# Kernel tuning notes

Hardware: AMD Instinct MI355X
Metric: run time of the kernel (lower is better)

Reference implementation:

```python
import jax, jax.numpy as jnp
import numpy as np

N = 100000
E = 1600000
IN_C = 128
HID = 64


def setup_inputs() -> dict:
    key = jax.random.key(0)
    ks = jax.random.split(key, 8)
    x = jax.random.normal(ks[0], (N, IN_C), dtype=jnp.float32)
    edge_index = jax.random.randint(ks[1], (2, E), 0, N, dtype=jnp.int64)
    # Glorot-ish init for faithfulness; exact init values don't matter for correctness baseline
    W1 = jax.random.normal(ks[2], (IN_C, HID), dtype=jnp.float32) / np.sqrt(IN_C)
    b1 = jnp.zeros((HID,), dtype=jnp.float32)
    W2 = jax.random.normal(ks[3], (HID, HID), dtype=jnp.float32) / np.sqrt(HID)
    b2 = jnp.zeros((HID,), dtype=jnp.float32)
    Wc = jax.random.normal(ks[4], (HID, 1), dtype=jnp.float32) / np.sqrt(HID)
    bc = jnp.zeros((1,), dtype=jnp.float32)
    return {"x": x, "edge_index": edge_index, "W1": W1, "b1": b1,
            "W2": W2, "b2": b2, "Wc": Wc, "bc": bc}


def _gcn_conv(x, W, b, src, dst, norm, n_nodes):
    # PyG GCNConv: h = x @ W; out[dst] += norm * h[src]; out += b
    h = x @ W                                  # [N, out_c]
    msg = h[src] * norm[:, None]               # [E+N, out_c] gather + scale
    out = jax.ops.segment_sum(msg, dst, num_segments=n_nodes)  # scatter-add
    return out + b


def reference(x, edge_index, W1, b1, W2, b2, Wc, bc):
    n = x.shape[0]
    loop = jnp.arange(n, dtype=edge_index.dtype)
    src = jnp.concatenate([edge_index[0], loop])   # add self-loops (PyG default)
    dst = jnp.concatenate([edge_index[1], loop])
    # symmetric normalization: deg over destination (col) including self-loops
    deg = jax.ops.segment_sum(jnp.ones_like(dst, dtype=x.dtype), dst, num_segments=n)
    dinv = jnp.where(deg > 0, jax.lax.rsqrt(deg), 0.0)
    norm = dinv[src] * dinv[dst]                   # [E+N]

    h = jax.nn.relu(_gcn_conv(x, W1, b1, src, dst, norm, n))
    h = jax.nn.relu(_gcn_conv(h, W2, b2, src, dst, norm, n))
    logits = (h @ Wc + bc)[:, 0]                   # squeeze(-1)
    return logits
```

## Files before the change

kernel.cpp:

```cpp
#include <hip/hip_runtime.h>
#include <hip/hip_fp16.h>


#define IN_C 128
#define HID  64
#define CAP  64
#define NBUCKET 256
#define BCHUNK  391
#define BUCKET_CAP 8192
#define EPB 2048

typedef __attribute__((ext_vector_type(4))) _Float16 half4;
typedef __attribute__((ext_vector_type(8))) _Float16 half8;
typedef __attribute__((ext_vector_type(4))) float f32x4;

__global__ void k_zero_i32(int* __restrict__ p, int n) {
    int i = blockIdx.x * blockDim.x + threadIdx.x;
    if (i < n) p[i] = 0;
}

__global__ void k_partition(const int* __restrict__ ei, int* __restrict__ cursor,
                            int2* __restrict__ ebuf, int E) {
    __shared__ int2 stage[EPB];
    __shared__ unsigned char sbkt[EPB];
    __shared__ int cnt[NBUCKET];
    __shared__ int pfx[NBUCKET];
    __shared__ int bstart[NBUCKET];
    __shared__ int gbase[NBUCKET];

    int t = threadIdx.x;
    int e0 = blockIdx.x * EPB;
    cnt[t] = 0;
    __syncthreads();

    int  myb[EPB / 256];
    int2 myv[EPB / 256];
    #pragma unroll
    for (int i = 0; i < EPB / 256; ++i) {
        int e = e0 + i * 256 + t;
        int b = -1; int2 v = make_int2(0, 0);
        if (e < E) {
            v.x = ei[e];
            v.y = ei[E + e];
            b = v.y / BCHUNK;
            atomicAdd(&cnt[b], 1);
        }
        myb[i] = b; myv[i] = v;
    }
    __syncthreads();

    int c = cnt[t];
    pfx[t] = c;
    __syncthreads();
    #pragma unroll
    for (int off = 1; off < NBUCKET; off <<= 1) {
        int u = (t >= off) ? pfx[t - off] : 0;
        __syncthreads();
        pfx[t] += u;
        __syncthreads();
    }
    bstart[t] = pfx[t] - c;
    gbase[t]  = atomicAdd(&cursor[t], c);
    cnt[t] = 0;
    __syncthreads();

    #pragma unroll
    for (int i = 0; i < EPB / 256; ++i) {
        int b = myb[i];
        if (b >= 0) {
            int pos = bstart[b] + atomicAdd(&cnt[b], 1);
            stage[pos] = myv[i];
            sbkt[pos]  = (unsigned char)b;
        }
    }
    __syncthreads();

    int total = pfx[NBUCKET - 1];
    for (int i = t; i < total; i += 256) {
        int b = sbkt[i];
        int off = gbase[b] + (i - bstart[b]);
        if (off < BUCKET_CAP)
            ebuf[(long)b * BUCKET_CAP + off] = stage[i];
    }
}

__global__ void k_fill_bucket(const int2* __restrict__ ebuf, const int* __restrict__ cursor,
                              int* __restrict__ deg, float* __restrict__ dinv,
                              int* __restrict__ pairs, int n) {
    __shared__ int lcur[BCHUNK];
    int t = threadIdx.x;
    int b = blockIdx.x;
    int lo = b * BCHUNK;
    int hi = min(n, lo + BCHUNK);
    for (int i = t; i < BCHUNK; i += 256) lcur[i] = 0;
    __syncthreads();

    int cnt = min(cursor[b], BUCKET_CAP);
    const int2* p = ebuf + (long)b * BUCKET_CAP;
    for (int i = t; i < cnt; i += 256) {
        int2 v = p[i];
        int pos = atomicAdd(&lcur[v.y - lo], 1);
        if (pos < CAP) pairs[(long)v.y * CAP + pos] = v.x;
    }
    __syncthreads();
    for (int i = lo + t; i < hi; i += 256) {
        int d = lcur[i - lo];
        deg[i]  = d;
        dinv[i] = rsqrtf((float)(d + 1));
    }
}

__launch_bounds__(256)
__global__ void k_gemm1_mfma(const float* __restrict__ X, const float* __restrict__ W,
                             const float* __restrict__ dinv, _Float16* __restrict__ H,
                             int n) {
    int lane = threadIdx.x & 63;
    int m    = lane & 15;
    int quad = lane >> 4;
    int wid  = blockIdx.x * (blockDim.x >> 6) + (threadIdx.x >> 6);
    int nwav = gridDim.x * (blockDim.x >> 6);

    half8 wf[4][4];
    #pragma unroll
    for (int ks = 0; ks < 4; ++ks)
        #pragma unroll
        for (int ct = 0; ct < 4; ++ct)
            #pragma unroll
            for (int j = 0; j < 8; ++j)
                wf[ct][ks][j] = (_Float16)W[(ks * 32 + quad * 8 + j) * 64 + ct * 16 + m];

    int ntile = (n + 15) >> 4;
    for (int tile = wid; tile < ntile; tile += nwav) {
        int row0 = tile << 4;
        const float* xr = X + (long)min(row0 + m, n - 1) * IN_C;

        float4 xa[4], xb[4];
        #pragma unroll
        for (int ks = 0; ks < 4; ++ks) {
            xa[ks] = *(const float4*)&xr[ks * 32 + quad * 8];
            xb[ks] = *(const float4*)&xr[ks * 32 + quad * 8 + 4];
        }
        half8 af[4];
        #pragma unroll
        for (int ks = 0; ks < 4; ++ks) {
            af[ks][0] = (_Float16)xa[ks].x; af[ks][1] = (_Float16)xa[ks].y;
            af[ks][2] = (_Float16)xa[ks].z; af[ks][3] = (_Float16)xa[ks].w;
            af[ks][4] = (_Float16)xb[ks].x; af[ks][5] = (_Float16)xb[ks].y;
            af[ks][6] = (_Float16)xb[ks].z; af[ks][7] = (_Float16)xb[ks].w;
        }

        f32x4 acc0 = {0.f, 0.f, 0.f, 0.f}, acc1 = acc0, acc2 = acc0, acc3 = acc0;
        #pragma unroll
        for (int ks = 0; ks < 4; ++ks) {
            acc0 = __builtin_amdgcn_mfma_f32_16x16x32_f16(af[ks], wf[0][ks], acc0, 0, 0, 0);
            acc1 = __builtin_amdgcn_mfma_f32_16x16x32_f16(af[ks], wf[1][ks], acc1, 0, 0, 0);
            acc2 = __builtin_amdgcn_mfma_f32_16x16x32_f16(af[ks], wf[2][ks], acc2, 0, 0, 0);
            acc3 = __builtin_amdgcn_mfma_f32_16x16x32_f16(af[ks], wf[3][ks], acc3, 0, 0, 0);
        }

        #pragma unroll
        for (int r = 0; r < 4; ++r) {
            int row = row0 + quad * 4 + r;
            if (row < n) {
                float dv = dinv[row];
                _Float16* hp = H + (long)row * 64 + m;
                hp[0]  = (_Float16)(dv * acc0[r]);
                hp[16] = (_Float16)(dv * acc1[r]);
                hp[32] = (_Float16)(dv * acc2[r]);
                hp[48] = (_Float16)(dv * acc3[r]);
            }
        }
    }
}

__device__ __forceinline__ float4 gather_sum(const _Float16* __restrict__ H,
                                             int4 q, int cnt, int gb, int c4,
                                             float4 acc) {
    int jj = 0;
    for (; jj + 8 <= cnt; jj += 8) {
        int sl = gb + (jj >> 2);
        int a0 = __shfl(q.x, sl, 64),     a1 = __shfl(q.y, sl, 64);
        int a2 = __shfl(q.z, sl, 64),     a3 = __shfl(q.w, sl, 64);
        int b0 = __shfl(q.x, sl + 1, 64), b1 = __shfl(q.y, sl + 1, 64);
        int b2 = __shfl(q.z, sl + 1, 64), b3 = __shfl(q.w, sl + 1, 64);
        half4 v0 = *(const half4*)&H[(long)a0 * 64 + c4];
        half4 v1 = *(const half4*)&H[(long)a1 * 64 + c4];
        half4 v2 = *(const half4*)&H[(long)a2 * 64 + c4];
        half4 v3 = *(const half4*)&H[(long)a3 * 64 + c4];
        half4 v4 = *(const half4*)&H[(long)b0 * 64 + c4];
        half4 v5 = *(const half4*)&H[(long)b1 * 64 + c4];
        half4 v6 = *(const half4*)&H[(long)b2 * 64 + c4];
        half4 v7 = *(const half4*)&H[(long)b3 * 64 + c4];
        acc.x += (float)v0.x + (float)v1.x + (float)v2.x + (float)v3.x
               + (float)v4.x + (float)v5.x + (float)v6.x + (float)v7.x;
        acc.y += (float)v0.y + (float)v1.y + (float)v2.y + (float)v3.y
               + (float)v4.y + (float)v5.y + (float)v6.y + (float)v7.y;
        acc.z += (float)v0.z + (float)v1.z + (float)v2.z + (float)v3.z
               + (float)v4.z + (float)v5.z + (float)v6.z + (float)v7.z;
        acc.w += (float)v0.w + (float)v1.w + (float)v2.w + (float)v3.w
               + (float)v4.w + (float)v5.w + (float)v6.w + (float)v7.w;
    }
    if (jj < cnt) {
        int sl = gb + (jj >> 2);
        int s[8];
        s[0] = __shfl(q.x, sl, 64);     s[1] = __shfl(q.y, sl, 64);
        s[2] = __shfl(q.z, sl, 64);     s[3] = __shfl(q.w, sl, 64);
        s[4] = __shfl(q.x, sl + 1, 64); s[5] = __shfl(q.y, sl + 1, 64);
        s[6] = __shfl(q.z, sl + 1, 64); s[7] = __shfl(q.w, sl + 1, 64);
        #pragma unroll
        for (int u = 0; u < 8; ++u) {
            bool ok = (jj + u) < cnt;
            int sc = ok ? s[u] : 0;
            half4 v = *(const half4*)&H[(long)sc * 64 + c4];
            float w = ok ? 1.f : 0.f;
            acc.x = fmaf((float)v.x, w, acc.x);
            acc.y = fmaf((float)v.y, w, acc.y);
            acc.z = fmaf((float)v.z, w, acc.z);
            acc.w = fmaf((float)v.w, w, acc.w);
        }
    }
    return acc;
}

__global__ void k_gather_fuse(const _Float16* __restrict__ H, const int* __restrict__ pairs,
                              const int* __restrict__ deg, const float* __restrict__ dinv,
                              const float* __restrict__ b1, const float* __restrict__ W2,
                              _Float16* __restrict__ OUT, int n) {
    __shared__ float Ws[64 * 64];
    for (int i = threadIdx.x * 4; i < 64 * 64; i += 256 * 4)
        *(float4*)&Ws[i] = *(const float4*)&W2[i];
    __syncthreads();

    int t = blockIdx.x * blockDim.x + threadIdx.x;
    int node = t >> 4;
    int l16  = threadIdx.x & 15;
    int gb   = (threadIdx.x & 63) & ~15;
    if (node >= n) return;
    int c4 = l16 * 4;

    float di = dinv[node];
    int cnt  = min(deg[node], CAP);
    int4 q = *(const int4*)&pairs[(long)node * CAP + l16 * 4];

    half4 h0 = *(const half4*)&H[(long)node * 64 + c4];
    float4 acc = make_float4((float)h0.x, (float)h0.y, (float)h0.z, (float)h0.w);
    acc = gather_sum(H, q, cnt, gb, c4, acc);

    float4 bb = *(const float4*)&b1[c4];
    float4 r = make_float4(fmaxf(fmaf(di, acc.x, bb.x), 0.f),
                           fmaxf(fmaf(di, acc.y, bb.y), 0.f),
                           fmaxf(fmaf(di, acc.z, bb.z), 0.f),
                           fmaxf(fmaf(di, acc.w, bb.w), 0.f));
    float4 o = make_float4(0.f, 0.f, 0.f, 0.f);
    #pragma unroll
    for (int j = 0; j < 16; ++j) {
        float4 bv;
        bv.x = __shfl(r.x, j, 16); bv.y = __shfl(r.y, j, 16);
        bv.z = __shfl(r.z, j, 16); bv.w = __shfl(r.w, j, 16);
        float4 w0 = *(const float4*)&Ws[(j * 4 + 0) * 64 + c4];
        float4 w1 = *(const float4*)&Ws[(j * 4 + 1) * 64 + c4];
        float4 w2 = *(const float4*)&Ws[(j * 4 + 2) * 64 + c4];
        float4 w3 = *(const float4*)&Ws[(j * 4 + 3) * 64 + c4];
        o.x = fmaf(bv.x, w0.x, o.x); o.y = fmaf(bv.x, w0.y, o.y);
        o.z = fmaf(bv.x, w0.z, o.z); o.w = fmaf(bv.x, w0.w, o.w);
        o.x = fmaf(bv.y, w1.x, o.x); o.y = fmaf(bv.y, w1.y, o.y);
        o.z = fmaf(bv.y, w1.z, o.z); o.w = fmaf(bv.y, w1.w, o.w);
        o.x = fmaf(bv.z, w2.x, o.x); o.y = fmaf(bv.z, w2.y, o.y);
        o.z = fmaf(bv.z, w2.z, o.z); o.w = fmaf(bv.z, w2.w, o.w);
        o.x = fmaf(bv.w, w3.x, o.x); o.y = fmaf(bv.w, w3.y, o.y);
        o.z = fmaf(bv.w, w3.z, o.z); o.w = fmaf(bv.w, w3.w, o.w);
    }
    half4 ho;
    ho.x = (_Float16)(di * o.x); ho.y = (_Float16)(di * o.y);
    ho.z = (_Float16)(di * o.z); ho.w = (_Float16)(di * o.w);
    *(half4*)&OUT[(long)node * 64 + c4] = ho;
}

__global__ void k_gather_head(const _Float16* __restrict__ H, const int* __restrict__ pairs,
                              const int* __restrict__ deg, const float* __restrict__ dinv,
                              const float* __restrict__ b2, const float* __restrict__ Wc,
                              const float* __restrict__ bc, float* __restrict__ OUT, int n) {
    int t = blockIdx.x * blockDim.x + threadIdx.x;
    int node = t >> 4;
    int l16  = threadIdx.x & 15;
    int gb   = (threadIdx.x & 63) & ~15;
    if (node >= n) return;
    int c4 = l16 * 4;

    float di = dinv[node];
    int cnt  = min(deg[node], CAP);
    int4 q = *(const int4*)&pairs[(long)node * CAP + l16 * 4];

    half4 h0 = *(const half4*)&H[(long)node * 64 + c4];
    float4 acc = make_float4((float)h0.x, (float)h0.y, (float)h0.z, (float)h0.w);
    acc = gather_sum(H, q, cnt, gb, c4, acc);

    float4 bb = *(const float4*)&b2[c4];
    float4 wc = *(const float4*)&Wc[c4];
    float v = fmaxf(fmaf(di, acc.x, bb.x), 0.f) * wc.x +
              fmaxf(fmaf(di, acc.y, bb.y), 0.f) * wc.y +
              fmaxf(fmaf(di, acc.z, bb.z), 0.f) * wc.z +
              fmaxf(fmaf(di, acc.w, bb.w), 0.f) * wc.w;
    v += __shfl_down(v, 8, 16);
    v += __shfl_down(v, 4, 16);
    v += __shfl_down(v, 2, 16);
    v += __shfl_down(v, 1, 16);
    if (l16 == 0) OUT[node] = v + bc[0];
}

extern "C" void kernel_launch(void* const* d_in, const int* in_sizes, int n_in,
                              void* d_out, int out_size, void* d_ws, size_t ws_size,
                              hipStream_t stream) {
    const float* x  = (const float*)d_in[0];
    const int*   ei = (const int*)d_in[1];
    const float* W1 = (const float*)d_in[2];
    const float* b1 = (const float*)d_in[3];
    const float* W2 = (const float*)d_in[4];
    const float* b2 = (const float*)d_in[5];
    const float* Wc = (const float*)d_in[6];
    const float* bc = (const float*)d_in[7];
    float* out = (float*)d_out;

    const int n = in_sizes[0] / IN_C;
    const int E = in_sizes[1] / 2;

    char* w = (char*)d_ws;
    auto alloc = [&](size_t bytes) { char* r = w; w += (bytes + 255) & ~(size_t)255; return r; };
    int*      deg    = (int*)alloc((size_t)n * 4);
    float*    dinv   = (float*)alloc((size_t)n * 4);
    int*      pairs  = (int*)alloc((size_t)n * CAP * 4);
    _Float16* A16    = (_Float16*)alloc((size_t)n * HID * 2);
    _Float16* B16    = (_Float16*)alloc((size_t)n * HID * 2);
    int*      cursor = (int*)alloc(NBUCKET * 4);
    int2*     ebuf   = (int2*)alloc((size_t)NBUCKET * BUCKET_CAP * 8);

    const int BS = 256;
    dim3 blk(BS);
    auto grid_items = [&](long items) { return dim3((unsigned)((items + BS - 1) / BS)); };

    k_zero_i32<<<dim3(1), blk, 0, stream>>>(cursor, NBUCKET);
    k_partition<<<dim3((unsigned)((E + EPB - 1) / EPB)), blk, 0, stream>>>(ei, cursor, ebuf, E);
    k_fill_bucket<<<dim3(NBUCKET), blk, 0, stream>>>(ebuf, cursor, deg, dinv, pairs, n);

    k_gemm1_mfma<<<dim3(1024), blk, 0, stream>>>(x, W1, dinv, A16, n);

    k_gather_fuse<<<grid_items((long)n * 16), blk, 0, stream>>>(
        A16, pairs, deg, dinv, b1, W2, B16, n);

    k_gather_head<<<grid_items((long)n * 16), blk, 0, stream>>>(
        B16, pairs, deg, dinv, b2, Wc, bc, out, n);
}
```

Measured before the change: 227.9 us.

## Pack edge keys to 32 bits, pad neighbor lists, gather two nodes per group

The edge partition buffer now stores a packed 32-bit key (source shifted by 9 bits, local destination in the low bits) instead of an int2, which halves the partition traffic. Neighbor lists are padded to a multiple of 8 with a sentinel index pointing to an extra zeroed row in the feature buffers, so the gather no longer needs a masked tail loop. Each 16-lane group now processes two nodes at once, which doubles the independent loads in flight and shares the W2 reads from shared memory. The cost is higher register pressure, half as many threads, and extra sentinel loads for low-degree nodes.

New measurement: 607.0 us. 2.66x slower.

```diff
diff --git a/kernel.cpp b/kernel.cpp
--- a/kernel.cpp
+++ b/kernel.cpp
@@ -14,14 +14,19 @@
 typedef __attribute__((ext_vector_type(8))) _Float16 half8;
 typedef __attribute__((ext_vector_type(4))) float f32x4;
 
-__global__ void k_zero_i32(int* __restrict__ p, int n) {
-    int i = blockIdx.x * blockDim.x + threadIdx.x;
-    if (i < n) p[i] = 0;
+__global__ void k_init(int* __restrict__ cursor, _Float16* __restrict__ A16,
+                       _Float16* __restrict__ B16, int n) {
+    int t = threadIdx.x;
+    if (t < NBUCKET) cursor[t] = 0;
+    if (t < 64) {
+        A16[(long)n * 64 + t] = (_Float16)0.f;
+        B16[(long)n * 64 + t] = (_Float16)0.f;
+    }
 }
 
 __global__ void k_partition(const int* __restrict__ ei, int* __restrict__ cursor,
-                            int2* __restrict__ ebuf, int E) {
-    __shared__ int2 stage[EPB];
+                            unsigned* __restrict__ ebuf, int E) {
+    __shared__ unsigned stage[EPB];
     __shared__ unsigned char sbkt[EPB];
     __shared__ int cnt[NBUCKET];
     __shared__ int pfx[NBUCKET];
@@ -33,19 +38,20 @@
     cnt[t] = 0;
     __syncthreads();
 
-    int  myb[EPB / 256];
-    int2 myv[EPB / 256];
+    int      myb[EPB / 256];
+    unsigned myk[EPB / 256];
     #pragma unroll
     for (int i = 0; i < EPB / 256; ++i) {
         int e = e0 + i * 256 + t;
-        int b = -1; int2 v = make_int2(0, 0);
+        int b = -1; unsigned k = 0;
         if (e < E) {
-            v.x = ei[e];
-            v.y = ei[E + e];
-            b = v.y / BCHUNK;
+            int s = ei[e];
+            int d = ei[E + e];
+            b = d / BCHUNK;
+            k = ((unsigned)s << 9) | (unsigned)(d - b * BCHUNK);
             atomicAdd(&cnt[b], 1);
         }
-        myb[i] = b; myv[i] = v;
+        myb[i] = b; myk[i] = k;
     }
     __syncthreads();
 
@@ -69,7 +75,7 @@
         int b = myb[i];
         if (b >= 0) {
             int pos = bstart[b] + atomicAdd(&cnt[b], 1);
-            stage[pos] = myv[i];
+            stage[pos] = myk[i];
             sbkt[pos]  = (unsigned char)b;
         }
     }
@@ -84,7 +90,7 @@
     }
 }
 
-__global__ void k_fill_bucket(const int2* __restrict__ ebuf, const int* __restrict__ cursor,
+__global__ void k_fill_bucket(const unsigned* __restrict__ ebuf, const int* __restrict__ cursor,
                               int* __restrict__ deg, float* __restrict__ dinv,
                               int* __restrict__ pairs, int n) {
     __shared__ int lcur[BCHUNK];
@@ -96,17 +102,22 @@
     __syncthreads();
 
     int cnt = min(cursor[b], BUCKET_CAP);
-    const int2* p = ebuf + (long)b * BUCKET_CAP;
+    const unsigned* p = ebuf + (long)b * BUCKET_CAP;
     for (int i = t; i < cnt; i += 256) {
-        int2 v = p[i];
-        int pos = atomicAdd(&lcur[v.y - lo], 1);
-        if (pos < CAP) pairs[(long)v.y * CAP + pos] = v.x;
+        unsigned k = p[i];
+        int dl  = k & 511;
+        int src = k >> 9;
+        int pos = atomicAdd(&lcur[dl], 1);
+        if (pos < CAP) pairs[(long)(lo + dl) * CAP + pos] = src;
     }
     __syncthreads();
     for (int i = lo + t; i < hi; i += 256) {
         int d = lcur[i - lo];
         deg[i]  = d;
         dinv[i] = rsqrtf((float)(d + 1));
+        int dc = min(d, CAP);
+        int cp = max(8, (dc + 7) & ~7);
+        for (int s = dc; s < cp; ++s) pairs[(long)i * CAP + s] = n;
     }
 }
 
@@ -173,53 +184,53 @@
     }
 }
 
-__device__ __forceinline__ float4 gather_sum(const _Float16* __restrict__ H,
-                                             int4 q, int cnt, int gb, int c4,
-                                             float4 acc) {
-    int jj = 0;
-    for (; jj + 8 <= cnt; jj += 8) {
-        int sl = gb + (jj >> 2);
-        int a0 = __shfl(q.x, sl, 64),     a1 = __shfl(q.y, sl, 64);
-        int a2 = __shfl(q.z, sl, 64),     a3 = __shfl(q.w, sl, 64);
-        int b0 = __shfl(q.x, sl + 1, 64), b1 = __shfl(q.y, sl + 1, 64);
-        int b2 = __shfl(q.z, sl + 1, 64), b3 = __shfl(q.w, sl + 1, 64);
-        half4 v0 = *(const half4*)&H[(long)a0 * 64 + c4];
-        half4 v1 = *(const half4*)&H[(long)a1 * 64 + c4];
-        half4 v2 = *(const half4*)&H[(long)a2 * 64 + c4];
-        half4 v3 = *(const half4*)&H[(long)a3 * 64 + c4];
-        half4 v4 = *(const half4*)&H[(long)b0 * 64 + c4];
-        half4 v5 = *(const half4*)&H[(long)b1 * 64 + c4];
-        half4 v6 = *(const half4*)&H[(long)b2 * 64 + c4];
-        half4 v7 = *(const half4*)&H[(long)b3 * 64 + c4];
-        acc.x += (float)v0.x + (float)v1.x + (float)v2.x + (float)v3.x
-               + (float)v4.x + (float)v5.x + (float)v6.x + (float)v7.x;
-        acc.y += (float)v0.y + (float)v1.y + (float)v2.y + (float)v3.y
-               + (float)v4.y + (float)v5.y + (float)v6.y + (float)v7.y;
-        acc.z += (float)v0.z + (float)v1.z + (float)v2.z + (float)v3.z
-               + (float)v4.z + (float)v5.z + (float)v6.z + (float)v7.z;
-        acc.w += (float)v0.w + (float)v1.w + (float)v2.w + (float)v3.w
-               + (float)v4.w + (float)v5.w + (float)v6.w + (float)v7.w;
-    }
-    if (jj < cnt) {
-        int sl = gb + (jj >> 2);
-        int s[8];
-        s[0] = __shfl(q.x, sl, 64);     s[1] = __shfl(q.y, sl, 64);
-        s[2] = __shfl(q.z, sl, 64);     s[3] = __shfl(q.w, sl, 64);
-        s[4] = __shfl(q.x, sl + 1, 64); s[5] = __shfl(q.y, sl + 1, 64);
-        s[6] = __shfl(q.z, sl + 1, 64); s[7] = __shfl(q.w, sl + 1, 64);
-        #pragma unroll
-        for (int u = 0; u < 8; ++u) {
-            bool ok = (jj + u) < cnt;
-            int sc = ok ? s[u] : 0;
-            half4 v = *(const half4*)&H[(long)sc * 64 + c4];
-            float w = ok ? 1.f : 0.f;
-            acc.x = fmaf((float)v.x, w, acc.x);
-            acc.y = fmaf((float)v.y, w, acc.y);
-            acc.z = fmaf((float)v.z, w, acc.z);
-            acc.w = fmaf((float)v.w, w, acc.w);
-        }
-    }
-    return acc;
+#define CHUNK_SUM(q, sl, sx, sy, sz, sw)                                   \
+    {                                                                      \
+        int a0 = __shfl(q.x, sl, 64),     a1 = __shfl(q.y, sl, 64);        \
+        int a2 = __shfl(q.z, sl, 64),     a3 = __shfl(q.w, sl, 64);        \
+        int b0 = __shfl(q.x, sl + 1, 64), b1 = __shfl(q.y, sl + 1, 64);    \
+        int b2 = __shfl(q.z, sl + 1, 64), b3 = __shfl(q.w, sl + 1, 64);    \
+        half4 v0 = *(const half4*)&H[(long)a0 * 64 + c4];                  \
+        half4 v1 = *(const half4*)&H[(long)a1 * 64 + c4];                  \
+        half4 v2 = *(const half4*)&H[(long)a2 * 64 + c4];                  \
+        half4 v3 = *(const half4*)&H[(long)a3 * 64 + c4];                  \
+        half4 v4 = *(const half4*)&H[(long)b0 * 64 + c4];                  \
+        half4 v5 = *(const half4*)&H[(long)b1 * 64 + c4];                  \
+        half4 v6 = *(const half4*)&H[(long)b2 * 64 + c4];                  \
+        half4 v7 = *(const half4*)&H[(long)b3 * 64 + c4];                  \
+        sx = (float)v0.x + (float)v1.x + (float)v2.x + (float)v3.x         \
+           + (float)v4.x + (float)v5.x + (float)v6.x + (float)v7.x;        \
+        sy = (float)v0.y + (float)v1.y + (float)v2.y + (float)v3.y         \
+           + (float)v4.y + (float)v5.y + (float)v6.y + (float)v7.y;        \
+        sz = (float)v0.z + (float)v1.z + (float)v2.z + (float)v3.z         \
+           + (float)v4.z + (float)v5.z + (float)v6.z + (float)v7.z;        \
+        sw = (float)v0.w + (float)v1.w + (float)v2.w + (float)v3.w         \
+           + (float)v4.w + (float)v5.w + (float)v6.w + (float)v7.w;        \
+    }
+
+__device__ __forceinline__ void gather2(const _Float16* __restrict__ H,
+                                        int4 q0, int4 q1, int cp0, int cp1,
+                                        int gb, int c4, float4& acc0, float4& acc1) {
+    int m = max(cp0, cp1);
+    for (int jj = 0; jj < m; jj += 8) {
+        int j0 = min(jj, cp0 - 8);
+        int j1 = min(jj, cp1 - 8);
+        float w0 = (jj < cp0) ? 1.f : 0.f;
+        float w1 = (jj < cp1) ? 1.f : 0.f;
+        int sl0 = gb + (j0 >> 2);
+        int sl1 = gb + (j1 >> 2);
+        float s0x, s0y, s0z, s0w, s1x, s1y, s1z, s1w;
+        CHUNK_SUM(q0, sl0, s0x, s0y, s0z, s0w);
+        CHUNK_SUM(q1, sl1, s1x, s1y, s1z, s1w);
+        acc0.x = fmaf(s0x, w0, acc0.x); acc0.y = fmaf(s0y, w0, acc0.y);
+        acc0.z = fmaf(s0z, w0, acc0.z); acc0.w = fmaf(s0w, w0, acc0.w);
+        acc1.x = fmaf(s1x, w1, acc1.x); acc1.y = fmaf(s1y, w1, acc1.y);
+        acc1.z = fmaf(s1z, w1, acc1.z); acc1.w = fmaf(s1w, w1, acc1.w);
+    }
+}
+
+__device__ __forceinline__ int padded_cnt(int d) {
+    return max(8, (min(d, CAP) + 7) & ~7);
 }
 
 __global__ void k_gather_fuse(const _Float16* __restrict__ H, const int* __restrict__ pairs,
@@ -231,81 +242,122 @@
         *(float4*)&Ws[i] = *(const float4*)&W2[i];
     __syncthreads();
 
-    int t = blockIdx.x * blockDim.x + threadIdx.x;
-    int node = t >> 4;
-    int l16  = threadIdx.x & 15;
-    int gb   = (threadIdx.x & 63) & ~15;
-    if (node >= n) return;
+    int g   = (blockIdx.x * blockDim.x + threadIdx.x) >> 4;
+    int l16 = threadIdx.x & 15;
+    int gb  = (threadIdx.x & 63) & ~15;
+    int node0 = g * 2;
+    if (node0 >= n) return;
+    bool has1 = (node0 + 1) < n;
+    int node1 = has1 ? node0 + 1 : node0;
     int c4 = l16 * 4;
 
-    float di = dinv[node];
-    int cnt  = min(deg[node], CAP);
-    int4 q = *(const int4*)&pairs[(long)node * CAP + l16 * 4];
-
-    half4 h0 = *(const half4*)&H[(long)node * 64 + c4];
-    float4 acc = make_float4((float)h0.x, (float)h0.y, (float)h0.z, (float)h0.w);
-    acc = gather_sum(H, q, cnt, gb, c4, acc);
+    float di0 = dinv[node0], di1 = dinv[node1];
+    int cp0 = padded_cnt(deg[node0]);
+    int cp1 = padded_cnt(deg[node1]);
+    int4 q0 = *(const int4*)&pairs[(long)node0 * CAP + l16 * 4];
+    int4 q1 = *(const int4*)&pairs[(long)node1 * CAP + l16 * 4];
+
+    half4 h0 = *(const half4*)&H[(long)node0 * 64 + c4];
+    half4 h1 = *(const half4*)&H[(long)node1 * 64 + c4];
+    float4 acc0 = make_float4((float)h0.x, (float)h0.y, (float)h0.z, (float)h0.w);
+    float4 acc1 = make_float4((float)h1.x, (float)h1.y, (float)h1.z, (float)h1.w);
+    gather2(H, q0, q1, cp0, cp1, gb, c4, acc0, acc1);
 
     float4 bb = *(const float4*)&b1[c4];
-    float4 r = make_float4(fmaxf(fmaf(di, acc.x, bb.x), 0.f),
-                           fmaxf(fmaf(di, acc.y, bb.y), 0.f),
-                           fmaxf(fmaf(di, acc.z, bb.z), 0.f),
-                           fmaxf(fmaf(di, acc.w, bb.w), 0.f));
-    float4 o = make_float4(0.f, 0.f, 0.f, 0.f);
+    float4 r0 = make_float4(fmaxf(fmaf(di0, acc0.x, bb.x), 0.f),
+                            fmaxf(fmaf(di0, acc0.y, bb.y), 0.f),
+                            fmaxf(fmaf(di0, acc0.z, bb.z), 0.f),
+                            fmaxf(fmaf(di0, acc0.w, bb.w), 0.f));
+    float4 r1 = make_float4(fmaxf(fmaf(di1, acc1.x, bb.x), 0.f),
+                            fmaxf(fmaf(di1, acc1.y, bb.y), 0.f),
+                            fmaxf(fmaf(di1, acc1.z, bb.z), 0.f),
+                            fmaxf(fmaf(di1, acc1.w, bb.w), 0.f));
+    float4 o0 = make_float4(0.f, 0.f, 0.f, 0.f);
+    float4 o1 = o0;
     #pragma unroll
     for (int j = 0; j < 16; ++j) {
-        float4 bv;
-        bv.x = __shfl(r.x, j, 16); bv.y = __shfl(r.y, j, 16);
-        bv.z = __shfl(r.z, j, 16); bv.w = __shfl(r.w, j, 16);
+        float4 bv0, bv1;
+        bv0.x = __shfl(r0.x, j, 16); bv0.y = __shfl(r0.y, j, 16);
+        bv0.z = __shfl(r0.z, j, 16); bv0.w = __shfl(r0.w, j, 16);
+        bv1.x = __shfl(r1.x, j, 16); bv1.y = __shfl(r1.y, j, 16);
+        bv1.z = __shfl(r1.z, j, 16); bv1.w = __shfl(r1.w, j, 16);
         float4 w0 = *(const float4*)&Ws[(j * 4 + 0) * 64 + c4];
         float4 w1 = *(const float4*)&Ws[(j * 4 + 1) * 64 + c4];
         float4 w2 = *(const float4*)&Ws[(j * 4 + 2) * 64 + c4];
         float4 w3 = *(const float4*)&Ws[(j * 4 + 3) * 64 + c4];
-        o.x = fmaf(bv.x, w0.x, o.x); o.y = fmaf(bv.x, w0.y, o.y);
-        o.z = fmaf(bv.x, w0.z, o.z); o.w = fmaf(bv.x, w0.w, o.w);
-        o.x = fmaf(bv.y, w1.x, o.x); o.y = fmaf(bv.y, w1.y, o.y);
-        o.z = fmaf(bv.y, w1.z, o.z); o.w = fmaf(bv.y, w1.w, o.w);
-        o.x = fmaf(bv.z, w2.x, o.x); o.y = fmaf(bv.z, w2.y, o.y);
-        o.z = fmaf(bv.z, w2.z, o.z); o.w = fmaf(bv.z, w2.w, o.w);
-        o.x = fmaf(bv.w, w3.x, o.x); o.y = fmaf(bv.w, w3.y, o.y);
-        o.z = fmaf(bv.w, w3.z, o.z); o.w = fmaf(bv.w, w3.w, o.w);
+        o0.x = fmaf(bv0.x, w0.x, o0.x); o0.y = fmaf(bv0.x, w0.y, o0.y);
+        o0.z = fmaf(bv0.x, w0.z, o0.z); o0.w = fmaf(bv0.x, w0.w, o0.w);
+        o0.x = fmaf(bv0.y, w1.x, o0.x); o0.y = fmaf(bv0.y, w1.y, o0.y);
+        o0.z = fmaf(bv0.y, w1.z, o0.z); o0.w = fmaf(bv0.y, w1.w, o0.w);
+        o0.x = fmaf(bv0.z, w2.x, o0.x); o0.y = fmaf(bv0.z, w2.y, o0.y);
+        o0.z = fmaf(bv0.z, w2.z, o0.z); o0.w = fmaf(bv0.z, w2.w, o0.w);
+        o0.x = fmaf(bv0.w, w3.x, o0.x); o0.y = fmaf(bv0.w, w3.y, o0.y);
+        o0.z = fmaf(bv0.w, w3.z, o0.z); o0.w = fmaf(bv0.w, w3.w, o0.w);
+        o1.x = fmaf(bv1.x, w0.x, o1.x); o1.y = fmaf(bv1.x, w0.y, o1.y);
+        o1.z = fmaf(bv1.x, w0.z, o1.z); o1.w = fmaf(bv1.x, w0.w, o1.w);
+        o1.x = fmaf(bv1.y, w1.x, o1.x); o1.y = fmaf(bv1.y, w1.y, o1.y);
+        o1.z = fmaf(bv1.y, w1.z, o1.z); o1.w = fmaf(bv1.y, w1.w, o1.w);
+        o1.x = fmaf(bv1.z, w2.x, o1.x); o1.y = fmaf(bv1.z, w2.y, o1.y);
+        o1.z = fmaf(bv1.z, w2.z, o1.z); o1.w = fmaf(bv1.z, w2.w, o1.w);
+        o1.x = fmaf(bv1.w, w3.x, o1.x); o1.y = fmaf(bv1.w, w3.y, o1.y);
+        o1.z = fmaf(bv1.w, w3.z, o1.z); o1.w = fmaf(bv1.w, w3.w, o1.w);
     }
     half4 ho;
-    ho.x = (_Float16)(di * o.x); ho.y = (_Float16)(di * o.y);
-    ho.z = (_Float16)(di * o.z); ho.w = (_Float16)(di * o.w);
-    *(half4*)&OUT[(long)node * 64 + c4] = ho;
+    ho.x = (_Float16)(di0 * o0.x); ho.y = (_Float16)(di0 * o0.y);
+    ho.z = (_Float16)(di0 * o0.z); ho.w = (_Float16)(di0 * o0.w);
+    *(half4*)&OUT[(long)node0 * 64 + c4] = ho;
+    if (has1) {
+        ho.x = (_Float16)(di1 * o1.x); ho.y = (_Float16)(di1 * o1.y);
+        ho.z = (_Float16)(di1 * o1.z); ho.w = (_Float16)(di1 * o1.w);
+        *(half4*)&OUT[(long)node1 * 64 + c4] = ho;
+    }
 }
 
 __global__ void k_gather_head(const _Float16* __restrict__ H, const int* __restrict__ pairs,
                               const int* __restrict__ deg, const float* __restrict__ dinv,
                               const float* __restrict__ b2, const float* __restrict__ Wc,
                               const float* __restrict__ bc, float* __restrict__ OUT, int n) {
-    int t = blockIdx.x * blockDim.x + threadIdx.x;
-    int node = t >> 4;
-    int l16  = threadIdx.x & 15;
-    int gb   = (threadIdx.x & 63) & ~15;
-    if (node >= n) return;
+    int g   = (blockIdx.x * blockDim.x + threadIdx.x) >> 4;
+    int l16 = threadIdx.x & 15;
+    int gb  = (threadIdx.x & 63) & ~15;
+    int node0 = g * 2;
+    if (node0 >= n) return;
+    bool has1 = (node0 + 1) < n;
+    int node1 = has1 ? node0 + 1 : node0;
     int c4 = l16 * 4;
 
-    float di = dinv[node];
-    int cnt  = min(deg[node], CAP);
-    int4 q = *(const int4*)&pairs[(long)node * CAP + l16 * 4];
-
-    half4 h0 = *(const half4*)&H[(long)node * 64 + c4];
-    float4 acc = make_float4((float)h0.x, (float)h0.y, (float)h0.z, (float)h0.w);
-    acc = gather_sum(H, q, cnt, gb, c4, acc);
+    float di0 = dinv[node0], di1 = dinv[node1];
+    int cp0 = padded_cnt(deg[node0]);
+    int cp1 = padded_cnt(deg[node1]);
+    int4 q0 = *(const int4*)&pairs[(long)node0 * CAP + l16 * 4];
+    int4 q1 = *(const int4*)&pairs[(long)node1 * CAP + l16 * 4];
+
+    half4 h0 = *(const half4*)&H[(long)node0 * 64 + c4];
+    half4 h1 = *(const half4*)&H[(long)node1 * 64 + c4];
+    float4 acc0 = make_float4((float)h0.x, (float)h0.y, (float)h0.z, (float)h0.w);
+    float4 acc1 = make_float4((float)h1.x, (float)h1.y, (float)h1.z, (float)h1.w);
+    gather2(H, q0, q1, cp0, cp1, gb, c4, acc0, acc1);
 
     float4 bb = *(const float4*)&b2[c4];
     float4 wc = *(const float4*)&Wc[c4];
-    float v = fmaxf(fmaf(di, acc.x, bb.x), 0.f) * wc.x +
-              fmaxf(fmaf(di, acc.y, bb.y), 0.f) * wc.y +
-              fmaxf(fmaf(di, acc.z, bb.z), 0.f) * wc.z +
-              fmaxf(fmaf(di, acc.w, bb.w), 0.f) * wc.w;
-    v += __shfl_down(v, 8, 16);
-    v += __shfl_down(v, 4, 16);
-    v += __shfl_down(v, 2, 16);
-    v += __shfl_down(v, 1, 16);
-    if (l16 == 0) OUT[node] = v + bc[0];
+    float v0 = fmaxf(fmaf(di0, acc0.x, bb.x), 0.f) * wc.x +
+               fmaxf(fmaf(di0, acc0.y, bb.y), 0.f) * wc.y +
+               fmaxf(fmaf(di0, acc0.z, bb.z), 0.f) * wc.z +
+               fmaxf(fmaf(di0, acc0.w, bb.w), 0.f) * wc.w;
+    float v1 = fmaxf(fmaf(di1, acc1.x, bb.x), 0.f) * wc.x +
+               fmaxf(fmaf(di1, acc1.y, bb.y), 0.f) * wc.y +
+               fmaxf(fmaf(di1, acc1.z, bb.z), 0.f) * wc.z +
+               fmaxf(fmaf(di1, acc1.w, bb.w), 0.f) * wc.w;
+    #pragma unroll
+    for (int off = 8; off > 0; off >>= 1) {
+        v0 += __shfl_down(v0, off, 16);
+        v1 += __shfl_down(v1, off, 16);
+    }
+    if (l16 == 0) {
+        float b = bc[0];
+        OUT[node0] = v0 + b;
+        if (has1) OUT[node0 + 1] = v1 + b;
+    }
 }
 
 extern "C" void kernel_launch(void* const* d_in, const int* in_sizes, int n_in,
@@ -329,24 +381,25 @@
     int*      deg    = (int*)alloc((size_t)n * 4);
     float*    dinv   = (float*)alloc((size_t)n * 4);
     int*      pairs  = (int*)alloc((size_t)n * CAP * 4);
-    _Float16* A16    = (_Float16*)alloc((size_t)n * HID * 2);
-    _Float16* B16    = (_Float16*)alloc((size_t)n * HID * 2);
+    _Float16* A16    = (_Float16*)alloc((size_t)(n + 1) * HID * 2);
+    _Float16* B16    = (_Float16*)alloc((size_t)(n + 1) * HID * 2);
     int*      cursor = (int*)alloc(NBUCKET * 4);
-    int2*     ebuf   = (int2*)alloc((size_t)NBUCKET * BUCKET_CAP * 8);
+    unsigned* ebuf   = (unsigned*)alloc((size_t)NBUCKET * BUCKET_CAP * 4);
 
     const int BS = 256;
     dim3 blk(BS);
     auto grid_items = [&](long items) { return dim3((unsigned)((items + BS - 1) / BS)); };
 
-    k_zero_i32<<<dim3(1), blk, 0, stream>>>(cursor, NBUCKET);
+    k_init<<<dim3(1), blk, 0, stream>>>(cursor, A16, B16, n);
     k_partition<<<dim3((unsigned)((E + EPB - 1) / EPB)), blk, 0, stream>>>(ei, cursor, ebuf, E);
     k_fill_bucket<<<dim3(NBUCKET), blk, 0, stream>>>(ebuf, cursor, deg, dinv, pairs, n);
 
     k_gemm1_mfma<<<dim3(1024), blk, 0, stream>>>(x, W1, dinv, A16, n);
 
-    k_gather_fuse<<<grid_items((long)n * 16), blk, 0, stream>>>(
+    long groups = (n + 1) / 2;
+    k_gather_fuse<<<grid_items(groups * 16), blk, 0, stream>>>(
         A16, pairs, deg, dinv, b1, W2, B16, n);
 
-    k_gather_head<<<grid_items((long)n * 16), blk, 0, stream>>>(
+    k_gather_head<<<grid_items(groups * 16), blk, 0, stream>>>(
         B16, pairs, deg, dinv, b2, Wc, bc, out, n);
 }
```

## Pack edge keys to 32-bit and pad neighbor lists with zero-row sentinel

Applied to the files above, without the earlier changes.

Edges are packed as (src<<9 | local dst) into one 32-bit word, which halves the bucket-buffer traffic between partition and fill. Neighbor lists are padded to a multiple of 16 with a sentinel index that points at an extra zeroed row in each feature buffer. This lets the gather loop run 16 loads per iteration with no predicated tail. The cost is extra wasted gathers of the zero row for nodes whose degree is not a multiple of 16, plus the padding writes.

New measurement: 229.3 us. About the same (+0.6%).

```diff
diff --git a/kernel.cpp b/kernel.cpp
--- a/kernel.cpp
+++ b/kernel.cpp
@@ -14,14 +14,19 @@
 typedef __attribute__((ext_vector_type(8))) _Float16 half8;
 typedef __attribute__((ext_vector_type(4))) float f32x4;
 
-__global__ void k_zero_i32(int* __restrict__ p, int n) {
-    int i = blockIdx.x * blockDim.x + threadIdx.x;
-    if (i < n) p[i] = 0;
+__global__ void k_init(int* __restrict__ cursor, _Float16* __restrict__ A16,
+                       _Float16* __restrict__ B16, int n) {
+    int t = threadIdx.x;
+    if (t < NBUCKET) cursor[t] = 0;
+    if (t < 64) {
+        A16[(long)n * 64 + t] = (_Float16)0.f;
+        B16[(long)n * 64 + t] = (_Float16)0.f;
+    }
 }
 
 __global__ void k_partition(const int* __restrict__ ei, int* __restrict__ cursor,
-                            int2* __restrict__ ebuf, int E) {
-    __shared__ int2 stage[EPB];
+                            unsigned* __restrict__ ebuf, int E) {
+    __shared__ unsigned stage[EPB];
     __shared__ unsigned char sbkt[EPB];
     __shared__ int cnt[NBUCKET];
     __shared__ int pfx[NBUCKET];
@@ -33,19 +38,20 @@
     cnt[t] = 0;
     __syncthreads();
 
-    int  myb[EPB / 256];
-    int2 myv[EPB / 256];
+    int      myb[EPB / 256];
+    unsigned myk[EPB / 256];
     #pragma unroll
     for (int i = 0; i < EPB / 256; ++i) {
         int e = e0 + i * 256 + t;
-        int b = -1; int2 v = make_int2(0, 0);
+        int b = -1; unsigned k = 0;
         if (e < E) {
-            v.x = ei[e];
-            v.y = ei[E + e];
-            b = v.y / BCHUNK;
+            int s = ei[e];
+            int d = ei[E + e];
+            b = d / BCHUNK;
+            k = ((unsigned)s << 9) | (unsigned)(d - b * BCHUNK);
             atomicAdd(&cnt[b], 1);
         }
-        myb[i] = b; myv[i] = v;
+        myb[i] = b; myk[i] = k;
     }
     __syncthreads();
 
@@ -69,7 +75,7 @@
         int b = myb[i];
         if (b >= 0) {
             int pos = bstart[b] + atomicAdd(&cnt[b], 1);
-            stage[pos] = myv[i];
+            stage[pos] = myk[i];
             sbkt[pos]  = (unsigned char)b;
         }
     }
@@ -84,7 +90,7 @@
     }
 }
 
-__global__ void k_fill_bucket(const int2* __restrict__ ebuf, const int* __restrict__ cursor,
+__global__ void k_fill_bucket(const unsigned* __restrict__ ebuf, const int* __restrict__ cursor,
                               int* __restrict__ deg, float* __restrict__ dinv,
                               int* __restrict__ pairs, int n) {
     __shared__ int lcur[BCHUNK];
@@ -96,17 +102,22 @@
     __syncthreads();
 
     int cnt = min(cursor[b], BUCKET_CAP);
-    const int2* p = ebuf + (long)b * BUCKET_CAP;
+    const unsigned* p = ebuf + (long)b * BUCKET_CAP;
     for (int i = t; i < cnt; i += 256) {
-        int2 v = p[i];
-        int pos = atomicAdd(&lcur[v.y - lo], 1);
-        if (pos < CAP) pairs[(long)v.y * CAP + pos] = v.x;
+        unsigned k = p[i];
+        int dl  = k & 511;
+        int src = k >> 9;
+        int pos = atomicAdd(&lcur[dl], 1);
+        if (pos < CAP) pairs[(long)(lo + dl) * CAP + pos] = src;
     }
     __syncthreads();
     for (int i = lo + t; i < hi; i += 256) {
         int d = lcur[i - lo];
-        deg[i]  = d;
         dinv[i] = rsqrtf((float)(d + 1));
+        int dc = min(d, CAP);
+        int cp = max(16, (dc + 15) & ~15);
+        deg[i] = cp;
+        for (int s = dc; s < cp; ++s) pairs[(long)i * CAP + s] = n;
     }
 }
 
@@ -174,50 +185,50 @@
 }
 
 __device__ __forceinline__ float4 gather_sum(const _Float16* __restrict__ H,
-                                             int4 q, int cnt, int gb, int c4,
+                                             int4 q, int cp, int gb, int c4,
                                              float4 acc) {
-    int jj = 0;
-    for (; jj + 8 <= cnt; jj += 8) {
+    for (int jj = 0; jj < cp; jj += 16) {
         int sl = gb + (jj >> 2);
         int a0 = __shfl(q.x, sl, 64),     a1 = __shfl(q.y, sl, 64);
         int a2 = __shfl(q.z, sl, 64),     a3 = __shfl(q.w, sl, 64);
         int b0 = __shfl(q.x, sl + 1, 64), b1 = __shfl(q.y, sl + 1, 64);
         int b2 = __shfl(q.z, sl + 1, 64), b3 = __shfl(q.w, sl + 1, 64);
-        half4 v0 = *(const half4*)&H[(long)a0 * 64 + c4];
-        half4 v1 = *(const half4*)&H[(long)a1 * 64 + c4];
-        half4 v2 = *(const half4*)&H[(long)a2 * 64 + c4];
-        half4 v3 = *(const half4*)&H[(long)a3 * 64 + c4];
-        half4 v4 = *(const half4*)&H[(long)b0 * 64 + c4];
-        half4 v5 = *(const half4*)&H[(long)b1 * 64 + c4];
-        half4 v6 = *(const half4*)&H[(long)b2 * 64 + c4];
-        half4 v7 = *(const half4*)&H[(long)b3 * 64 + c4];
-        acc.x += (float)v0.x + (float)v1.x + (float)v2.x + (float)v3.x
-               + (float)v4.x + (float)v5.x + (float)v6.x + (float)v7.x;
-        acc.y += (float)v0.y + (float)v1.y + (float)v2.y + (float)v3.y
-               + (float)v4.y + (float)v5.y + (float)v6.y + (float)v7.y;
-        acc.z += (float)v0.z + (float)v1.z + (float)v2.z + (float)v3.z
-               + (float)v4.z + (float)v5.z + (float)v6.z + (float)v7.z;
-        acc.w += (float)v0.w + (float)v1.w + (float)v2.w + (float)v3.w
-               + (float)v4.w + (float)v5.w + (float)v6.w + (float)v7.w;
-    }
-    if (jj < cnt) {
-        int sl = gb + (jj >> 2);
-        int s[8];
-        s[0] = __shfl(q.x, sl, 64);     s[1] = __shfl(q.y, sl, 64);
-        s[2] = __shfl(q.z, sl, 64);     s[3] = __shfl(q.w, sl, 64);
-        s[4] = __shfl(q.x, sl + 1, 64); s[5] = __shfl(q.y, sl + 1, 64);
-        s[6] = __shfl(q.z, sl + 1, 64); s[7] = __shfl(q.w, sl + 1, 64);
-        #pragma unroll
-        for (int u = 0; u < 8; ++u) {
-            bool ok = (jj + u) < cnt;
-            int sc = ok ? s[u] : 0;
-            half4 v = *(const half4*)&H[(long)sc * 64 + c4];
-            float w = ok ? 1.f : 0.f;
-            acc.x = fmaf((float)v.x, w, acc.x);
-            acc.y = fmaf((float)v.y, w, acc.y);
-            acc.z = fmaf((float)v.z, w, acc.z);
-            acc.w = fmaf((float)v.w, w, acc.w);
-        }
+        int c0 = __shfl(q.x, sl + 2, 64), c1 = __shfl(q.y, sl + 2, 64);
+        int c2 = __shfl(q.z, sl + 2, 64), c3 = __shfl(q.w, sl + 2, 64);
+        int d0 = __shfl(q.x, sl + 3, 64), d1 = __shfl(q.y, sl + 3, 64);
+        int d2 = __shfl(q.z, sl + 3, 64), d3 = __shfl(q.w, sl + 3, 64);
+        half4 v0  = *(const half4*)&H[(long)a0 * 64 + c4];
+        half4 v1  = *(const half4*)&H[(long)a1 * 64 + c4];
+        half4 v2  = *(const half4*)&H[(long)a2 * 64 + c4];
+        half4 v3  = *(const half4*)&H[(long)a3 * 64 + c4];
+        half4 v4  = *(const half4*)&H[(long)b0 * 64 + c4];
+        half4 v5  = *(const half4*)&H[(long)b1 * 64 + c4];
+        half4 v6  = *(const half4*)&H[(long)b2 * 64 + c4];
+        half4 v7  = *(const half4*)&H[(long)b3 * 64 + c4];
+        half4 v8  = *(const half4*)&H[(long)c0 * 64 + c4];
+        half4 v9  = *(const half4*)&H[(long)c1 * 64 + c4];
+        half4 v10 = *(const half4*)&H[(long)c2 * 64 + c4];
+        half4 v11 = *(const half4*)&H[(long)c3 * 64 + c4];
+        half4 v12 = *(const half4*)&H[(long)d0 * 64 + c4];
+        half4 v13 = *(const half4*)&H[(long)d1 * 64 + c4];
+        half4 v14 = *(const half4*)&H[(long)d2 * 64 + c4];
+        half4 v15 = *(const half4*)&H[(long)d3 * 64 + c4];
+        acc.x += (((float)v0.x + (float)v1.x) + ((float)v2.x + (float)v3.x))
+               + (((float)v4.x + (float)v5.x) + ((float)v6.x + (float)v7.x))
+               + (((float)v8.x + (float)v9.x) + ((float)v10.x + (float)v11.x))
+               + (((float)v12.x + (float)v13.x) + ((float)v14.x + (float)v15.x));
+        acc.y += (((float)v0.y + (float)v1.y) + ((float)v2.y + (float)v3.y))
+               + (((float)v4.y + (float)v5.y) + ((float)v6.y + (float)v7.y))
+               + (((float)v8.y + (float)v9.y) + ((float)v10.y + (float)v11.y))
+               + (((float)v12.y + (float)v13.y) + ((float)v14.y + (float)v15.y));
+        acc.z += (((float)v0.z + (float)v1.z) + ((float)v2.z + (float)v3.z))
+               + (((float)v4.z + (float)v5.z) + ((float)v6.z + (float)v7.z))
+               + (((float)v8.z + (float)v9.z) + ((float)v10.z + (float)v11.z))
+               + (((float)v12.z + (float)v13.z) + ((float)v14.z + (float)v15.z));
+        acc.w += (((float)v0.w + (float)v1.w) + ((float)v2.w + (float)v3.w))
+               + (((float)v4.w + (float)v5.w) + ((float)v6.w + (float)v7.w))
+               + (((float)v8.w + (float)v9.w) + ((float)v10.w + (float)v11.w))
+               + (((float)v12.w + (float)v13.w) + ((float)v14.w + (float)v15.w));
     }
     return acc;
 }
@@ -239,12 +250,12 @@
     int c4 = l16 * 4;
 
     float di = dinv[node];
-    int cnt  = min(deg[node], CAP);
+    int cp   = deg[node];
     int4 q = *(const int4*)&pairs[(long)node * CAP + l16 * 4];
 
     half4 h0 = *(const half4*)&H[(long)node * 64 + c4];
     float4 acc = make_float4((float)h0.x, (float)h0.y, (float)h0.z, (float)h0.w);
-    acc = gather_sum(H, q, cnt, gb, c4, acc);
+    acc = gather_sum(H, q, cp, gb, c4, acc);
 
     float4 bb = *(const float4*)&b1[c4];
     float4 r = make_float4(fmaxf(fmaf(di, acc.x, bb.x), 0.f),
@@ -288,12 +299,12 @@
     int c4 = l16 * 4;
 
     float di = dinv[node];
-    int cnt  = min(deg[node], CAP);
+    int cp   = deg[node];
     int4 q = *(const int4*)&pairs[(long)node * CAP + l16 * 4];
 
     half4 h0 = *(const half4*)&H[(long)node * 64 + c4];
     float4 acc = make_float4((float)h0.x, (float)h0.y, (float)h0.z, (float)h0.w);
-    acc = gather_sum(H, q, cnt, gb, c4, acc);
+    acc = gather_sum(H, q, cp, gb, c4, acc);
 
     float4 bb = *(const float4*)&b2[c4];
     float4 wc = *(const float4*)&Wc[c4];
@@ -329,16 +340,16 @@
     int*      deg    = (int*)alloc((size_t)n * 4);
     float*    dinv   = (float*)alloc((size_t)n * 4);
     int*      pairs  = (int*)alloc((size_t)n * CAP * 4);
-    _Float16* A16    = (_Float16*)alloc((size_t)n * HID * 2);
-    _Float16* B16    = (_Float16*)alloc((size_t)n * HID * 2);
+    _Float16* A16    = (_Float16*)alloc((size_t)(n + 1) * HID * 2);
+    _Float16* B16    = (_Float16*)alloc((size_t)(n + 1) * HID * 2);
     int*      cursor = (int*)alloc(NBUCKET * 4);
-    int2*     ebuf   = (int2*)alloc((size_t)NBUCKET * BUCKET_CAP * 8);
+    unsigned* ebuf   = (unsigned*)alloc((size_t)NBUCKET * BUCKET_CAP * 4);
 
     const int BS = 256;
     dim3 blk(BS);
     auto grid_items = [&](long items) { return dim3((unsigned)((items + BS - 1) / BS)); };
 
-    k_zero_i32<<<dim3(1), blk, 0, stream>>>(cursor, NBUCKET);
+    k_init<<<dim3(1), blk, 0, stream>>>(cursor, A16, B16, n);
     k_partition<<<dim3((unsigned)((E + EPB - 1) / EPB)), blk, 0, stream>>>(ei, cursor, ebuf, E);
     k_fill_bucket<<<dim3(NBUCKET), blk, 0, stream>>>(ebuf, cursor, deg, dinv, pairs, n);
 
```
